# Performance work log

Hardware: AMD Instinct MI355X
Metric: run time of the kernel (lower is better)

## Reference

```python
import jax, jax.numpy as jnp
import numpy as np

BN_EPS = 1e-5


def conv1x1(x, w, b):
    # x: [B,C,H,W], w: [O,C], b: [O] -> [B,O,H,W]
    return jnp.einsum('bchw,oc->bohw', x, w) + b[None, :, None, None]


def setup_inputs() -> dict:
    key = jax.random.key(0)
    ks = jax.random.split(key, 11)
    B, C, H, W = 8, 1024, 64, 32
    hid = 64  # C * rd_ratio (1/16)
    s = 0.02
    return {
        'x': jax.random.normal(ks[0], (B, C, H, W), dtype=jnp.float32),
        'theta_w': jax.random.normal(ks[1], (hid, C), dtype=jnp.float32) * s,
        'theta_b': jax.random.normal(ks[2], (hid,), dtype=jnp.float32) * s,
        'phi_w': jax.random.normal(ks[3], (hid, C), dtype=jnp.float32) * s,
        'phi_b': jax.random.normal(ks[4], (hid,), dtype=jnp.float32) * s,
        'g_w': jax.random.normal(ks[5], (hid, C), dtype=jnp.float32) * s,
        'g_b': jax.random.normal(ks[6], (hid,), dtype=jnp.float32) * s,
        'w_w': jax.random.normal(ks[7], (C, hid), dtype=jnp.float32) * s,
        'w_b': jax.random.normal(ks[8], (C,), dtype=jnp.float32) * s,
        'bn_gamma': jax.random.normal(ks[9], (C,), dtype=jnp.float32) * 0.1 + 1.0,
        'bn_beta': jax.random.normal(ks[10], (C,), dtype=jnp.float32) * 0.1,
    }


def reference(x, theta_w, theta_b, phi_w, phi_b, g_w, g_b, w_w, w_b, bn_gamma, bn_beta):
    B, C, H, W = x.shape
    hid = theta_w.shape[0]
    N = H * W
    theta = conv1x1(x, theta_w, theta_b).reshape(B, hid, N).transpose(0, 2, 1)  # [B,N,d]
    phi = conv1x1(x, phi_w, phi_b).reshape(B, hid, N)                           # [B,d,N]
    g = conv1x1(x, g_w, g_b).reshape(B, hid, N).transpose(0, 2, 1)              # [B,N,d]
    f = jnp.einsum('bnd,bdm->bnm', theta, phi) / N                              # [B,N,N]
    y = jnp.einsum('bnm,bmd->bnd', f, g)                                        # [B,N,d]
    y = y.transpose(0, 2, 1).reshape(B, hid, H, W)
    wy = conv1x1(y, w_w, w_b)                                                   # [B,C,H,W]
    # BatchNorm2d in training mode: batch statistics over (B,H,W), biased variance
    mean = wy.mean(axis=(0, 2, 3), keepdims=True)
    var = wy.var(axis=(0, 2, 3), keepdims=True)
    norm = (wy - mean) * jax.lax.rsqrt(var + BN_EPS)
    out = norm * bn_gamma[None, :, None, None] + bn_beta[None, :, None, None]
    return out + x
```

## Files before the change

kernel.cpp:

```cpp
#include <hip/hip_runtime.h>

#define B_    8
#define C_    1024
#define HID   64
#define N_    2048
#define RTOT  192

typedef __attribute__((ext_vector_type(8))) short   bf16x8;
typedef __attribute__((ext_vector_type(8))) unsigned short ush8;
typedef __attribute__((ext_vector_type(4))) unsigned short ush4;
typedef __attribute__((ext_vector_type(4))) float   f32x4;

#define WSB_WBF   ((size_t)0)
#define WSB_TPG   ((size_t)393216)
#define WSB_THT   ((size_t)6684672)
#define WSB_M     ((size_t)8781824)
#define WSB_G     ((size_t)8912896)
#define WSB_S     ((size_t)9043968)
#define WSB_WMBF  ((size_t)9046016)
#define WSB_SC    ((size_t)10094592)
#define WSB_SH    ((size_t)10098688)

static __device__ __forceinline__ unsigned short f2bf(float f) {
    union { float f; unsigned u; } v; v.f = f;
    unsigned r = v.u + 0x7fffu + ((v.u >> 16) & 1u);
    return (unsigned short)(r >> 16);
}
static __device__ __forceinline__ float bf2f(unsigned short h) {
    union { unsigned u; float f; } v; v.u = ((unsigned)h) << 16;
    return v.f;
}

__global__ __launch_bounds__(256) void wcvt(
    const float* __restrict__ tw, const float* __restrict__ pw,
    const float* __restrict__ gw, unsigned short* __restrict__ wbf)
{
    int idx = blockIdx.x * 256 + threadIdx.x;
    int r = idx >> 10, k = idx & 1023;
    float v = (r < 64) ? tw[(size_t)r * 1024 + k]
            : (r < 128) ? pw[(size_t)(r - 64) * 1024 + k]
                        : gw[(size_t)(r - 128) * 1024 + k];
    wbf[idx] = f2bf(v);
}

__global__ __launch_bounds__(512, 4) void proj_mfma(
    const float* __restrict__ x, const unsigned short* __restrict__ wbf,
    const float* __restrict__ tb, const float* __restrict__ pb,
    const float* __restrict__ gb, unsigned short* __restrict__ tpgbf,
    unsigned short* __restrict__ thT)
{
    const int b = blockIdx.y, n0 = blockIdx.x * 32;
    const int t = threadIdx.x, w = t >> 6, L = t & 63;
    const int og = w >> 1, nh = w & 1;
    const int lr = L & 15, q = L >> 4;
    __shared__ unsigned short A_lds[32][520];

    const float* xb = x + (size_t)b * C_ * N_ + n0;
    const unsigned short* bp = wbf + ((size_t)(48 * og + lr)) * 1024 + q * 8;

    f32x4 acc[3] = {};

#pragma unroll
    for (int ph = 0; ph < 2; ph++) {
        if (ph) __syncthreads();
#pragma unroll
        for (int i = 0; i < 4; i++) {
            int p = t + 512 * i;
            int n4 = p & 7;
            int c  = ((p >> 3) << 1);
            f32x4 v0 = *(const f32x4*)(xb + (size_t)(512 * ph + c) * N_ + n4 * 4);
            f32x4 v1 = *(const f32x4*)(xb + (size_t)(512 * ph + c + 1) * N_ + n4 * 4);
#pragma unroll
            for (int r = 0; r < 4; r++) {
                unsigned val = (unsigned)f2bf(v0[r]) | ((unsigned)f2bf(v1[r]) << 16);
                *(unsigned*)&A_lds[n4 * 4 + r][c] = val;
            }
        }
        __syncthreads();
#pragma unroll
        for (int ks = 0; ks < 16; ks++) {
            const int kg = ph * 512 + ks * 32;
            bf16x8 B0 = *(const bf16x8*)(bp + kg);
            bf16x8 B1 = *(const bf16x8*)(bp + 16 * 1024 + kg);
            bf16x8 B2 = *(const bf16x8*)(bp + 32 * 1024 + kg);
            bf16x8 A0 = *(const bf16x8*)&A_lds[16 * nh + lr][ks * 32 + q * 8];
            acc[0] = __builtin_amdgcn_mfma_f32_16x16x32_bf16(A0, B0, acc[0], 0, 0, 0);
            acc[1] = __builtin_amdgcn_mfma_f32_16x16x32_bf16(A0, B1, acc[1], 0, 0, 0);
            acc[2] = __builtin_amdgcn_mfma_f32_16x16x32_bf16(A0, B2, acc[2], 0, 0, 0);
        }
    }

#pragma unroll
    for (int j = 0; j < 3; j++) {
        int rcol = 48 * og + 16 * j + lr;
        float bias = (rcol < 64) ? tb[rcol]
                   : (rcol < 128) ? pb[rcol - 64] : gb[rcol - 128];
        ush4 o;
#pragma unroll
        for (int rr = 0; rr < 4; rr++) o[rr] = f2bf(acc[j][rr] + bias);
        *(ush4*)(tpgbf + ((size_t)b * RTOT + rcol) * N_ + n0 + 16 * nh + q * 4) = o;
        if (rcol < 64) {
#pragma unroll
            for (int rr = 0; rr < 4; rr++)
                thT[((size_t)b * N_ + n0 + 16 * nh + q * 4 + rr) * HID + rcol] = o[rr];
        }
    }
}

__global__ __launch_bounds__(256) void gram_mfma(
    const unsigned short* __restrict__ tpgbf, float* __restrict__ Mm,
    float* __restrict__ Gg, float* __restrict__ S)
{
    const int kc = blockIdx.x, p = blockIdx.y, b = blockIdx.z;
    const int t = threadIdx.x, w = t >> 6, L = t & 63;
    const int lr = L & 15, q = L >> 4;
    const unsigned short* base = tpgbf + (size_t)b * RTOT * N_;
    const unsigned short* Arow = base + (p ? 0 : (size_t)64 * N_);
    const unsigned short* Brow = base + (p ? 0 : (size_t)128 * N_);
    const unsigned short* ap = Arow + ((size_t)(16 * w + lr)) * N_ + kc * 128 + q * 8;
    const unsigned short* bp = Brow + ((size_t)lr) * N_ + kc * 128 + q * 8;

    bf16x8 ones;
#pragma unroll
    for (int j = 0; j < 8; j++) ones[j] = (short)0x3F80;

    f32x4 acc[4] = {};
    f32x4 accs = {};
#pragma unroll
    for (int it = 0; it < 4; ++it) {
        const int kn = it * 32;
        bf16x8 a = *(const bf16x8*)(ap + kn);
#pragma unroll
        for (int g = 0; g < 4; g++) {
            bf16x8 bb = *(const bf16x8*)(bp + (size_t)g * 16 * N_ + kn);
            acc[g] = __builtin_amdgcn_mfma_f32_16x16x32_bf16(a, bb, acc[g], 0, 0, 0);
        }
        if (p) accs = __builtin_amdgcn_mfma_f32_16x16x32_bf16(a, ones, accs, 0, 0, 0);
    }
    float* outp = (p ? Gg : Mm) + (size_t)b * HID * HID;
#pragma unroll
    for (int g = 0; g < 4; g++)
#pragma unroll
        for (int r = 0; r < 4; r++) {
            int row = 16 * w + q * 4 + r, col = 16 * g + lr;
            atomicAdd(outp + row * HID + col, acc[g][r]);
        }
    if (p && lr == 0) {
#pragma unroll
        for (int r = 0; r < 4; r++)
            atomicAdd(S + b * HID + 16 * w + q * 4 + r, accs[r]);
    }
}

__global__ __launch_bounds__(512) void wmstat(
    const float* __restrict__ ww, const float* __restrict__ Mm,
    const float* __restrict__ S, const float* __restrict__ G,
    const float* __restrict__ wb, const float* __restrict__ gamma,
    const float* __restrict__ beta, unsigned short* __restrict__ wmbf,
    float* __restrict__ scale, float* __restrict__ shift2)
{
    const int c = blockIdx.x;
    const int t = threadIdx.x;
    const int b = t >> 6, lane = t & 63;
    const float wbc = wb[c];
    const float* wr = ww + (size_t)c * HID;

    const float* mr = Mm + ((size_t)b * HID + lane) * HID;
    float acc = 0.f;
#pragma unroll
    for (int d = 0; d < HID; d += 4) {
        float4 m4 = *(const float4*)(mr + d);
        acc += wr[d] * m4.x + wr[d + 1] * m4.y + wr[d + 2] * m4.z + wr[d + 3] * m4.w;
    }
    unsigned short us = f2bf(acc * (1.0f / N_));
    wmbf[((size_t)b * C_ + c) * HID + lane] = us;
    float v = bf2f(us);
    float sv = S[b * HID + lane];
    float t1 = v * sv;
    for (int off = 32; off; off >>= 1) t1 += __shfl_down(t1, off);
    t1 = __shfl(t1, 0);
    const float* Gb = G + (size_t)b * HID * HID + (size_t)lane * HID;
    float inner = 0.f;
    for (int f = 0; f < HID; f++) inner = fmaf(Gb[f], __shfl(v, f), inner);
    float qq = v * inner;
    for (int off = 32; off; off >>= 1) qq += __shfl_down(qq, off);
    qq = __shfl(qq, 0);

    __shared__ float red[16];
    if (lane == 0) {
        red[b] = t1;
        red[8 + b] = qq + 2.f * wbc * t1;
    }
    __syncthreads();
    if (t == 0) {
        float asum = 0.f, asq = 0.f;
#pragma unroll
        for (int i = 0; i < 8; i++) { asum += red[i]; asq += red[8 + i]; }
        const float cnt = (float)B_ * (float)N_;
        const float inv = 1.0f / cnt;
        float mean = (asum + cnt * wbc) * inv;
        float e2   = (asq + cnt * wbc * wbc) * inv;
        float var  = e2 - mean * mean;
        float sc   = gamma[c] * rsqrtf(var + 1e-5f);
        scale[c]  = sc;
        shift2[c] = beta[c] - mean * sc + sc * wbc;
    }
}

__global__ __launch_bounds__(256) void finalk_mfma(
    const unsigned short* __restrict__ wmbf, const unsigned short* __restrict__ thT,
    const float* __restrict__ x, const float* __restrict__ scale,
    const float* __restrict__ shift2, float* __restrict__ out)
{
    const int b = blockIdx.z, c0 = blockIdx.y * 64, n0 = blockIdx.x * 64;
    const int t = threadIdx.x, w = t >> 6, L = t & 63;
    const int lr = L & 15, q = L >> 4;

    const unsigned short* ap = thT + ((size_t)b * N_ + n0 + 16 * w + lr) * HID + q * 8;
    const unsigned short* bp = wmbf + ((size_t)b * C_ + c0 + lr) * HID + q * 8;

    float4 xv[4];
    size_t xoff[4];
#pragma unroll
    for (int g = 0; g < 4; g++) {
        xoff[g] = ((size_t)b * C_ + c0 + 16 * g + lr) * N_ + n0 + 16 * w + q * 4;
        xv[g] = *(const float4*)(x + xoff[g]);
    }

    bf16x8 A0 = *(const bf16x8*)(ap);
    bf16x8 A1 = *(const bf16x8*)(ap + 32);
    f32x4 acc[4] = {};
#pragma unroll
    for (int g = 0; g < 4; g++) {
        bf16x8 Bg0 = *(const bf16x8*)(bp + (size_t)g * 16 * HID);
        bf16x8 Bg1 = *(const bf16x8*)(bp + (size_t)g * 16 * HID + 32);
        acc[g] = __builtin_amdgcn_mfma_f32_16x16x32_bf16(A0, Bg0, acc[g], 0, 0, 0);
        acc[g] = __builtin_amdgcn_mfma_f32_16x16x32_bf16(A1, Bg1, acc[g], 0, 0, 0);
    }
#pragma unroll
    for (int g = 0; g < 4; g++) {
        int c = c0 + 16 * g + lr;
        float sc = scale[c], sh = shift2[c];
        float4 o;
        o.x = fmaf(sc, acc[g][0], sh) + xv[g].x;
        o.y = fmaf(sc, acc[g][1], sh) + xv[g].y;
        o.z = fmaf(sc, acc[g][2], sh) + xv[g].z;
        o.w = fmaf(sc, acc[g][3], sh) + xv[g].w;
        *(float4*)(out + xoff[g]) = o;
    }
}

extern "C" void kernel_launch(void* const* d_in, const int* in_sizes, int n_in,
                              void* d_out, int out_size, void* d_ws, size_t ws_size,
                              hipStream_t stream)
{
    const float* x  = (const float*)d_in[0];
    const float* tw = (const float*)d_in[1];
    const float* tb = (const float*)d_in[2];
    const float* pw = (const float*)d_in[3];
    const float* pb = (const float*)d_in[4];
    const float* gw = (const float*)d_in[5];
    const float* gb = (const float*)d_in[6];
    const float* ww = (const float*)d_in[7];
    const float* wb = (const float*)d_in[8];
    const float* gamma = (const float*)d_in[9];
    const float* beta  = (const float*)d_in[10];
    float* out = (float*)d_out;

    char* ws = (char*)d_ws;
    unsigned short* wbf   = (unsigned short*)(ws + WSB_WBF);
    unsigned short* tpgbf = (unsigned short*)(ws + WSB_TPG);
    unsigned short* thT   = (unsigned short*)(ws + WSB_THT);
    float* Mm   = (float*)(ws + WSB_M);
    float* Gg   = (float*)(ws + WSB_G);
    float* S    = (float*)(ws + WSB_S);
    unsigned short* wmbf = (unsigned short*)(ws + WSB_WMBF);
    float* scl  = (float*)(ws + WSB_SC);
    float* shf  = (float*)(ws + WSB_SH);

    hipMemsetAsync(Mm, 0, (size_t)(2 * B_ * HID * HID + B_ * HID) * sizeof(float), stream);

    wcvt<<<dim3(RTOT * 1024 / 256), 256, 0, stream>>>(tw, pw, gw, wbf);
    proj_mfma<<<dim3(64, B_), 512, 0, stream>>>(x, wbf, tb, pb, gb, tpgbf, thT);
    gram_mfma<<<dim3(16, 2, B_), 256, 0, stream>>>(tpgbf, Mm, Gg, S);
    wmstat<<<C_, 512, 0, stream>>>(ww, Mm, S, Gg, wb, gamma, beta, wmbf, scl, shf);
    finalk_mfma<<<dim3(32, 16, B_), 256, 0, stream>>>(wmbf, thT, x, scl, shf, out);
}
```

Baseline: 235.8 us.

## Pre-transpose x to bf16 [B,N,C] and restructure projection GEMM tiling

Adds a separate transpose kernel that converts x to a bf16 token-major layout, so the projection kernel can load MFMA A operands straight from global memory without an LDS staging pass. The projection tile grows to 64 tokens with 6 accumulators per wave, and the grid halves to 256 blocks. The gram kernel doubles its K chunk per block, cutting atomic traffic, and the wmstat inner loop reads G with vector loads. The cost is an extra write and read of a 32 MB bf16 copy of x plus one more launch, and fewer blocks may leave CUs underused.

```diff
diff --git a/kernel.cpp b/kernel.cpp
--- a/kernel.cpp
+++ b/kernel.cpp
@@ -20,6 +20,7 @@
 #define WSB_WMBF  ((size_t)9046016)
 #define WSB_SC    ((size_t)10094592)
 #define WSB_SH    ((size_t)10098688)
+#define WSB_XT    ((size_t)10102784)
 
 static __device__ __forceinline__ unsigned short f2bf(float f) {
     union { float f; unsigned u; } v; v.f = f;
@@ -43,66 +44,82 @@
     wbf[idx] = f2bf(v);
 }
 
-__global__ __launch_bounds__(512, 4) void proj_mfma(
-    const float* __restrict__ x, const unsigned short* __restrict__ wbf,
+__global__ __launch_bounds__(256) void xpose(
+    const float* __restrict__ x, unsigned short* __restrict__ xT)
+{
+    const int n0 = blockIdx.x * 64, c0 = blockIdx.y * 64, b = blockIdx.z;
+    const int t = threadIdx.x;
+    __shared__ unsigned short tile[64][66];
+
+    const float* xb = x + ((size_t)b * C_ + c0) * N_ + n0;
+#pragma unroll
+    for (int p = 0; p < 2; p++) {
+        const int m  = t & 15;
+        const int cp = (t >> 4) + 16 * p;
+        const int cl = 2 * cp;
+        f32x4 v0 = *(const f32x4*)(xb + (size_t)cl * N_ + m * 4);
+        f32x4 v1 = *(const f32x4*)(xb + (size_t)(cl + 1) * N_ + m * 4);
+#pragma unroll
+        for (int r2 = 0; r2 < 4; r2++) {
+            unsigned val = (unsigned)f2bf(v0[r2]) | ((unsigned)f2bf(v1[r2]) << 16);
+            *(unsigned*)&tile[m * 4 + r2][cl] = val;
+        }
+    }
+    __syncthreads();
+    unsigned short* ob = xT + ((size_t)b * N_ + n0) * C_ + c0;
+#pragma unroll
+    for (int r = 0; r < 2; r++) {
+        const int nl   = (t >> 3) + 32 * r;
+        const int c8   = (t & 7) * 8;
+        uint4 u;
+        u.x = *(unsigned*)&tile[nl][c8];
+        u.y = *(unsigned*)&tile[nl][c8 + 2];
+        u.z = *(unsigned*)&tile[nl][c8 + 4];
+        u.w = *(unsigned*)&tile[nl][c8 + 6];
+        *(uint4*)(ob + (size_t)nl * C_ + c8) = u;
+    }
+}
+
+__global__ __launch_bounds__(512, 1) void proj_mfma(
+    const unsigned short* __restrict__ xT, const unsigned short* __restrict__ wbf,
     const float* __restrict__ tb, const float* __restrict__ pb,
     const float* __restrict__ gb, unsigned short* __restrict__ tpgbf,
     unsigned short* __restrict__ thT)
 {
-    const int b = blockIdx.y, n0 = blockIdx.x * 32;
+    const int b = blockIdx.y, n0 = blockIdx.x * 64;
     const int t = threadIdx.x, w = t >> 6, L = t & 63;
-    const int og = w >> 1, nh = w & 1;
+    const int nh = w & 3, rh = w >> 2;
     const int lr = L & 15, q = L >> 4;
-    __shared__ unsigned short A_lds[32][520];
-
-    const float* xb = x + (size_t)b * C_ * N_ + n0;
-    const unsigned short* bp = wbf + ((size_t)(48 * og + lr)) * 1024 + q * 8;
-
-    f32x4 acc[3] = {};
-
-#pragma unroll
-    for (int ph = 0; ph < 2; ph++) {
-        if (ph) __syncthreads();
-#pragma unroll
-        for (int i = 0; i < 4; i++) {
-            int p = t + 512 * i;
-            int n4 = p & 7;
-            int c  = ((p >> 3) << 1);
-            f32x4 v0 = *(const f32x4*)(xb + (size_t)(512 * ph + c) * N_ + n4 * 4);
-            f32x4 v1 = *(const f32x4*)(xb + (size_t)(512 * ph + c + 1) * N_ + n4 * 4);
-#pragma unroll
-            for (int r = 0; r < 4; r++) {
-                unsigned val = (unsigned)f2bf(v0[r]) | ((unsigned)f2bf(v1[r]) << 16);
-                *(unsigned*)&A_lds[n4 * 4 + r][c] = val;
-            }
-        }
-        __syncthreads();
-#pragma unroll
-        for (int ks = 0; ks < 16; ks++) {
-            const int kg = ph * 512 + ks * 32;
-            bf16x8 B0 = *(const bf16x8*)(bp + kg);
-            bf16x8 B1 = *(const bf16x8*)(bp + 16 * 1024 + kg);
-            bf16x8 B2 = *(const bf16x8*)(bp + 32 * 1024 + kg);
-            bf16x8 A0 = *(const bf16x8*)&A_lds[16 * nh + lr][ks * 32 + q * 8];
-            acc[0] = __builtin_amdgcn_mfma_f32_16x16x32_bf16(A0, B0, acc[0], 0, 0, 0);
-            acc[1] = __builtin_amdgcn_mfma_f32_16x16x32_bf16(A0, B1, acc[1], 0, 0, 0);
-            acc[2] = __builtin_amdgcn_mfma_f32_16x16x32_bf16(A0, B2, acc[2], 0, 0, 0);
-        }
-    }
-
-#pragma unroll
-    for (int j = 0; j < 3; j++) {
-        int rcol = 48 * og + 16 * j + lr;
+    const int nbase = n0 + nh * 16;
+
+    const unsigned short* ap = xT + ((size_t)b * N_ + nbase + lr) * C_ + q * 8;
+    const unsigned short* bp = wbf + ((size_t)(96 * rh + lr)) * 1024 + q * 8;
+
+    f32x4 acc[6] = {};
+#pragma unroll 4
+    for (int ks = 0; ks < 32; ks++) {
+        const int kg = ks * 32;
+        bf16x8 A = *(const bf16x8*)(ap + kg);
+#pragma unroll
+        for (int j = 0; j < 6; j++) {
+            bf16x8 Bj = *(const bf16x8*)(bp + (size_t)j * 16 * 1024 + kg);
+            acc[j] = __builtin_amdgcn_mfma_f32_16x16x32_bf16(A, Bj, acc[j], 0, 0, 0);
+        }
+    }
+
+#pragma unroll
+    for (int j = 0; j < 6; j++) {
+        int rcol = 96 * rh + 16 * j + lr;
         float bias = (rcol < 64) ? tb[rcol]
                    : (rcol < 128) ? pb[rcol - 64] : gb[rcol - 128];
         ush4 o;
 #pragma unroll
         for (int rr = 0; rr < 4; rr++) o[rr] = f2bf(acc[j][rr] + bias);
-        *(ush4*)(tpgbf + ((size_t)b * RTOT + rcol) * N_ + n0 + 16 * nh + q * 4) = o;
+        *(ush4*)(tpgbf + ((size_t)b * RTOT + rcol) * N_ + nbase + q * 4) = o;
         if (rcol < 64) {
 #pragma unroll
             for (int rr = 0; rr < 4; rr++)
-                thT[((size_t)b * N_ + n0 + 16 * nh + q * 4 + rr) * HID + rcol] = o[rr];
+                thT[((size_t)b * N_ + nbase + q * 4 + rr) * HID + rcol] = o[rr];
         }
     }
 }
@@ -117,8 +134,8 @@
     const unsigned short* base = tpgbf + (size_t)b * RTOT * N_;
     const unsigned short* Arow = base + (p ? 0 : (size_t)64 * N_);
     const unsigned short* Brow = base + (p ? 0 : (size_t)128 * N_);
-    const unsigned short* ap = Arow + ((size_t)(16 * w + lr)) * N_ + kc * 128 + q * 8;
-    const unsigned short* bp = Brow + ((size_t)lr) * N_ + kc * 128 + q * 8;
+    const unsigned short* ap = Arow + ((size_t)(16 * w + lr)) * N_ + kc * 256 + q * 8;
+    const unsigned short* bp = Brow + ((size_t)lr) * N_ + kc * 256 + q * 8;
 
     bf16x8 ones;
 #pragma unroll
@@ -127,7 +144,7 @@
     f32x4 acc[4] = {};
     f32x4 accs = {};
 #pragma unroll
-    for (int it = 0; it < 4; ++it) {
+    for (int it = 0; it < 8; ++it) {
         const int kn = it * 32;
         bf16x8 a = *(const bf16x8*)(ap + kn);
 #pragma unroll
@@ -179,9 +196,17 @@
     float t1 = v * sv;
     for (int off = 32; off; off >>= 1) t1 += __shfl_down(t1, off);
     t1 = __shfl(t1, 0);
-    const float* Gb = G + (size_t)b * HID * HID + (size_t)lane * HID;
+
+    const f32x4* Gb4 = (const f32x4*)(G + (size_t)b * HID * HID + (size_t)lane * HID);
     float inner = 0.f;
-    for (int f = 0; f < HID; f++) inner = fmaf(Gb[f], __shfl(v, f), inner);
+#pragma unroll
+    for (int fo = 0; fo < 16; fo++) {
+        f32x4 g4 = Gb4[fo];
+        inner = fmaf(g4[0], __shfl(v, 4 * fo + 0), inner);
+        inner = fmaf(g4[1], __shfl(v, 4 * fo + 1), inner);
+        inner = fmaf(g4[2], __shfl(v, 4 * fo + 2), inner);
+        inner = fmaf(g4[3], __shfl(v, 4 * fo + 3), inner);
+    }
     float qq = v * inner;
     for (int off = 32; off; off >>= 1) qq += __shfl_down(qq, off);
     qq = __shfl(qq, 0);
@@ -277,12 +302,14 @@
     unsigned short* wmbf = (unsigned short*)(ws + WSB_WMBF);
     float* scl  = (float*)(ws + WSB_SC);
     float* shf  = (float*)(ws + WSB_SH);
+    unsigned short* xT = (unsigned short*)(ws + WSB_XT);
 
     hipMemsetAsync(Mm, 0, (size_t)(2 * B_ * HID * HID + B_ * HID) * sizeof(float), stream);
 
     wcvt<<<dim3(RTOT * 1024 / 256), 256, 0, stream>>>(tw, pw, gw, wbf);
-    proj_mfma<<<dim3(64, B_), 512, 0, stream>>>(x, wbf, tb, pb, gb, tpgbf, thT);
-    gram_mfma<<<dim3(16, 2, B_), 256, 0, stream>>>(tpgbf, Mm, Gg, S);
+    xpose<<<dim3(32, 16, B_), 256, 0, stream>>>(x, xT);
+    proj_mfma<<<dim3(32, B_), 512, 0, stream>>>(xT, wbf, tb, pb, gb, tpgbf, thT);
+    gram_mfma<<<dim3(8, 2, B_), 256, 0, stream>>>(tpgbf, Mm, Gg, S);
     wmstat<<<C_, 512, 0, stream>>>(ww, Mm, S, Gg, wb, gamma, beta, wmbf, scl, shf);
     finalk_mfma<<<dim3(32, 16, B_), 256, 0, stream>>>(wmbf, thT, x, scl, shf, out);
 }
```

New measurement: 252.6 us. 7.2% more time.
